# Optimization experiments

Measured on AMD Instinct MI355X. Metric: run time of the kernel, lower is better.

Reference implementation:

```python
import jax, jax.numpy as jnp
import numpy as np

N, E, C, NB, NE, G = 20000, 320000, 64, 8, 4, 16
L2 = 9          # (max_ell+1)^2 with max_ell=2
RMAX = 5.0
HID = 16        # nonlinear readout hidden width


def setup_inputs():
    key = jax.random.key(0)
    ks = jax.random.split(key, 16)
    positions = jax.random.uniform(ks[0], (N, 3), dtype=jnp.float32) * 3.0
    elems = jax.random.randint(ks[1], (N,), 0, NE)
    node_attrs = jax.nn.one_hot(elems, NE, dtype=jnp.float32)
    edge_index = jax.random.randint(ks[2], (2, E), 0, N)
    batch = jnp.sort(jax.random.randint(ks[3], (N,), 0, G))
    shifts = jnp.zeros((E, 3), jnp.float32)
    atomic_energies = jnp.array([-1.0, -2.0, -3.0, -4.0], jnp.float32)
    sc = lambda k, shp, fan: jax.random.normal(k, shp, jnp.float32) / np.sqrt(fan).astype(np.float32)
    W_embed = sc(ks[4], (NE, C), NE)
    W_up = sc(ks[5], (2, C, C), C)
    W1 = sc(ks[6], (2, NB, 64), NB)
    W2 = sc(ks[7], (2, 64, C), 64)
    W_out = sc(ks[8], (2, C, C), C)
    W_skip = sc(ks[9], (2, NE, C), NE)
    w_read0 = sc(ks[10], (C,), C)
    W_r1 = sc(ks[11], (C, HID), C)
    w_r2 = sc(ks[12], (HID,), HID)
    return dict(positions=positions, node_attrs=node_attrs, shifts=shifts,
                atomic_energies=atomic_energies, W_embed=W_embed, W_up=W_up,
                W1=W1, W2=W2, W_out=W_out, W_skip=W_skip, w_read0=w_read0,
                W_r1=W_r1, w_r2=w_r2, edge_index=edge_index, batch=batch)


def _sph_harm_l2(u):
    # component-normalized real spherical harmonics up to l=2 on unit vectors
    x, y, z = u[:, 0], u[:, 1], u[:, 2]
    s3, s5, s15 = jnp.sqrt(3.0), jnp.sqrt(5.0), jnp.sqrt(15.0)
    return jnp.stack([jnp.ones_like(x),
                      s3 * x, s3 * y, s3 * z,
                      s15 * x * y, s15 * y * z, 0.5 * s5 * (3.0 * z * z - 1.0),
                      s15 * x * z, 0.5 * s15 * (x * x - y * y)], axis=-1)


def _radial(r):
    # Bessel radial basis with polynomial cutoff (p=6)
    n = jnp.arange(1, NB + 1, dtype=jnp.float32)
    rb = jnp.sqrt(2.0 / RMAX) * jnp.sin(n * jnp.pi * r[:, None] / RMAX) / r[:, None]
    u = r / RMAX
    fc = 1.0 - 28.0 * u**6 + 48.0 * u**7 - 21.0 * u**8
    fc = jnp.where(u < 1.0, fc, 0.0)
    return rb * fc[:, None]


def _energy_contributions(positions, node_attrs, shifts, atomic_energies,
                          W_embed, W_up, W1, W2, W_out, W_skip,
                          w_read0, W_r1, w_r2, edge_index, batch):
    snd, rcv = edge_index[0], edge_index[1]
    vec = positions[snd] - positions[rcv] + shifts                  # [E,3]
    r = jnp.sqrt(jnp.sum(vec * vec, axis=-1) + 1e-12)               # [E]
    Y = _sph_harm_l2(vec / r[:, None])                              # [E,L2]
    ef = _radial(r)                                                 # [E,NB]
    # E0: per-element reference energies, summed per graph
    e0 = jax.ops.segment_sum(node_attrs @ atomic_energies, batch, num_segments=G)
    h0 = node_attrs @ W_embed                                       # [N,C] scalar feats
    h = jnp.zeros((positions.shape[0], L2, C), h0.dtype).at[:, 0, :].set(h0)
    readouts = [lambda s: s @ w_read0,
                lambda s: jax.nn.silu(s @ W_r1) @ w_r2]             # linear / nonlinear
    energies = [e0]
    for i in range(2):
        hu = jnp.einsum('nlc,cd->nld', h, W_up[i])                  # channel mix
        R = jax.nn.silu(ef @ W1[i]) @ W2[i]                         # radial MLP [E,C]
        s = jnp.einsum('elc,el->ec', hu[snd], Y)                    # equivariant contraction
        m = Y[:, :, None] * (R * s)[:, None, :]                     # [E,L2,C] messages
        agg = jax.ops.segment_sum(m, rcv, num_segments=positions.shape[0])
        h = jnp.einsum('nlc,cd->nld', agg, W_out[i])
        h = h.at[:, 0, :].add(node_attrs @ W_skip[i])               # scalar skip connection
        node_en = readouts[i](h[:, 0, :])                           # [N]
        energies.append(jax.ops.segment_sum(node_en, batch, num_segments=G))
    return jnp.stack(energies, axis=-1)                             # [G, num_interactions+1]


def reference(positions, node_attrs, shifts, atomic_energies, W_embed, W_up,
              W1, W2, W_out, W_skip, w_read0, W_r1, w_r2, edge_index, batch):
    contributions = _energy_contributions(positions, node_attrs, shifts,
        atomic_energies, W_embed, W_up, W1, W2, W_out, W_skip,
        w_read0, W_r1, w_r2, edge_index, batch)
    total_energy = jnp.sum(contributions, axis=-1)                  # [G]
    forces = -jax.grad(lambda p: jnp.sum(_energy_contributions(p, node_attrs,
        shifts, atomic_energies, W_embed, W_up, W1, W2, W_out, W_skip,
        w_read0, W_r1, w_r2, edge_index, batch)))(positions)        # [N,3]
    return total_energy, contributions, forces
```

## Files before the change

### kernel.cpp

```cpp
#include <hip/hip_runtime.h>
#include <cmath>

constexpr int N_  = 20000;
constexpr int E_  = 320000;
constexpr int NE_ = 4;
constexpr int G_  = 16;
constexpr int CAP = 96;
constexpr int TAB = 4096;
constexpr float RMAXF = 5.0f;
constexpr float PI_F  = 3.14159265358979323846f;
constexpr float S3  = 1.7320508075688772f;
constexpr float S5  = 2.2360679774997896f;
constexpr float S15 = 3.8729833462074170f;
constexpr float KC_ = 0.6324555320336759f;

typedef unsigned short u16;
typedef unsigned int   u32;
typedef _Float16 f16;
typedef _Float16 f16x2 __attribute__((ext_vector_type(2)));

#define DEV static __device__ __forceinline__

__device__ float g_fallback[110000000];

DEV float sigmoidf_(float x){ return 1.0f/(1.0f+__expf(-x)); }

DEV float b2f(u16 u){ return __uint_as_float(((u32)u)<<16); }
DEV u16  f2b(float f){
  u32 x = __float_as_uint(f);
  return (u16)((x + 0x7FFFu + ((x>>16)&1u)) >> 16);
}
DEV u16  f2h(float f){ union{f16 h; u16 u;} v; v.h=(f16)f; return v.u; }
DEV float h2f(u16 u){ union{u16 u2; f16 h;} v; v.u2=u; return (float)v.h; }

DEV f16x2 u2h(u32 x){ union{u32 u; f16x2 h;} v; v.u=x; return v.h; }
DEV u32 h2u(f16x2 h){ union{u32 u; f16x2 h;} v; v.h=h; return v.u; }
DEV u32 pkh(float a, float b){ f16x2 h; h.x=(f16)a; h.y=(f16)b; return h2u(h); }

DEV void ld4(const float* __restrict__ p, float* d){
  float4 a = ((const float4*)p)[0];
  d[0]=a.x; d[1]=a.y; d[2]=a.z; d[3]=a.w;
}
DEV void ld4b(const u16* __restrict__ p, float* d){
  ushort4 a = *(const ushort4*)p;
  d[0]=b2f(a.x); d[1]=b2f(a.y); d[2]=b2f(a.z); d[3]=b2f(a.w);
}
DEV void ld4h(const u16* __restrict__ p, float* d){
  ushort4 a = *(const ushort4*)p;
  d[0]=h2f(a.x); d[1]=h2f(a.y); d[2]=h2f(a.z); d[3]=h2f(a.w);
}
DEV void st8b(u16* p, const float* d){
  uint4 v;
  v.x = (u32)f2b(d[0]) | ((u32)f2b(d[1])<<16);
  v.y = (u32)f2b(d[2]) | ((u32)f2b(d[3])<<16);
  v.z = (u32)f2b(d[4]) | ((u32)f2b(d[5])<<16);
  v.w = (u32)f2b(d[6]) | ((u32)f2b(d[7])<<16);
  *(uint4*)p = v;
}
DEV void st8h(u16* p, const float* d){
  uint4 v;
  v.x = pkh(d[0],d[1]); v.y = pkh(d[2],d[3]);
  v.z = pkh(d[4],d[5]); v.w = pkh(d[6],d[7]);
  *(uint4*)p = v;
}

__global__ void k_cnt(const int* __restrict__ ei, int* __restrict__ cntR){
  int e = blockIdx.x*256 + threadIdx.x;
  atomicAdd(&cntR[ei[E_+e]], 1);
}

__global__ void k_scan(const int* __restrict__ cntR, int* __restrict__ offR){
  __shared__ int part[256];
  int t = threadIdx.x;
  constexpr int CH = (N_+255)/256;
  int base = t*CH;
  int s=0;
  for (int i=0;i<CH;++i){ int idx=base+i; if(idx<N_) s+=cntR[idx]; }
  part[t]=s; __syncthreads();
  for (int d=1; d<256; d<<=1){
    int v = (t>=d)? part[t-d] : 0;
    __syncthreads();
    part[t]+=v;
    __syncthreads();
  }
  int run = (t==0)?0:part[t-1];
  for (int i=0;i<CH;++i){ int idx=base+i; if(idx<N_){ offR[idx]=run; run+=cntR[idx]; } }
  if (t==255) offR[N_]=run;
}

__global__ void k_perm(const int* __restrict__ ei, const int* __restrict__ offR,
                       int* __restrict__ cntR2, int* __restrict__ cntS,
                       int* __restrict__ pe, int* __restrict__ pSnd, int* __restrict__ pRcv,
                       int* __restrict__ listS){
  int e = blockIdx.x*256 + threadIdx.x;
  int s = ei[e], r = ei[E_+e];
  int p = offR[r] + atomicAdd(&cntR2[r], 1);
  pe[p] = e; pSnd[p] = s; pRcv[p] = r;
  int q = atomicAdd(&cntS[s], 1); if (q < CAP) listS[s*CAP+q] = p;
}

__global__ void k_pre(const float* __restrict__ Wout0, const float* __restrict__ Wup1,
                      const float* __restrict__ Wskip0, const float* __restrict__ wread0,
                      float* __restrict__ WA, float* __restrict__ sa,
                      float* __restrict__ va, float* __restrict__ sv){
  int t = threadIdx.x;
  for (int idx=t; idx<4096; idx+=256){
    int c = idx>>6, d = idx&63;
    float acc=0.f;
    for (int m=0;m<64;++m) acc += Wout0[c*64+m]*Wup1[m*64+d];
    WA[idx]=acc;
  }
  {
    int k = t>>6, d = t&63;
    float acc=0.f;
    for (int m=0;m<64;++m) acc += Wskip0[k*64+m]*Wup1[m*64+d];
    sa[t]=acc;
  }
  if (t<64){
    float acc=0.f;
    for (int d=0;d<64;++d) acc += Wout0[t*64+d]*wread0[d];
    va[t]=acc;
  }
  if (t<4){
    float acc=0.f;
    for (int d=0;d<64;++d) acc += Wskip0[t*64+d]*wread0[d];
    sv[t]=acc;
  }
}

__global__ __launch_bounds__(256, 2)
void k_rtab(const float* __restrict__ W1g, const float* __restrict__ W2g,
            u16* __restrict__ tab){
  __shared__ float sW1[1024];
  __shared__ u32   sW2h[4096];
  __shared__ u32   sAh[32*36];
  int t = threadIdx.x;
  for (int i=t;i<1024;i+=256) sW1[i]=W1g[i];
  for (int i=t;i<4096;i+=256){
    int L = i>>11, rem = i&2047, kp = rem>>6, c = rem&63;
    sW2h[i] = pkh(W2g[L*4096 + (2*kp)*64 + c], W2g[L*4096 + (2*kp+1)*64 + c]);
  }
  __syncthreads();
  int wid=t>>6, lane=t&63, q=lane>>3, j=lane&7, c0=j*8;
  int slot = wid*8 + q;
  int knot = blockIdx.x*32 + slot;
  bool valid = (knot <= TAB);
  float rad = fmaxf((float)knot * (RMAXF/(float)TAB), 1e-6f);
  float inv = 1.0f/rad;
  float tt = rad*(1.0f/RMAXF);
  float fc = 0.0f, dfc = 0.0f;
  if (tt < 1.0f){
    float t2=tt*tt, t4=t2*t2, t5=t4*tt, t6=t5*tt, t7=t6*tt, t8=t7*tt;
    fc  = 1.0f - 28.0f*t6 + 48.0f*t7 - 21.0f*t8;
    dfc = (-168.0f*t5 + 336.0f*t6 - 168.0f*t7)*(1.0f/RMAXF);
  }
  float th = rad*(PI_F/RMAXF);
  float s1 = __sinf(th), c1 = __cosf(th);
  float base = KC_*inv*fc;
  float efv[8], gfv[8];
  {
    float sb = s1, cb = c1;
    #pragma unroll
    for (int b=0;b<8;++b){
      efv[b] = base*sb;
      float wb_ = (float)(b+1)*(PI_F/RMAXF);
      float rb  = KC_*sb*inv;
      float drb = KC_*(wb_*cb - sb*inv)*inv;
      gfv[b] = drb*fc + rb*dfc;
      float sn = sb*c1 + cb*s1;
      cb = cb*c1 - sb*s1;
      sb = sn;
    }
  }
  u32* myAh = sAh + slot*36;
  for (int L=0; L<2; ++L){
    const float* w1 = sW1 + L*512;
    const u32*  w2h = sW2h + L*2048;
    float zz[8]={0,0,0,0,0,0,0,0};
    float wgv[8]={0,0,0,0,0,0,0,0};
    #pragma unroll 4
    for (int b=0;b<8;++b){
      float efb = efv[b], gfb = gfv[b];
      const float4* w=(const float4*)(w1 + b*64 + c0);
      float4 wa=w[0], wb=w[1];
      zz[0]+=efb*wa.x; zz[1]+=efb*wa.y; zz[2]+=efb*wa.z; zz[3]+=efb*wa.w;
      zz[4]+=efb*wb.x; zz[5]+=efb*wb.y; zz[6]+=efb*wb.z; zz[7]+=efb*wb.w;
      wgv[0]+=gfb*wa.x; wgv[1]+=gfb*wa.y; wgv[2]+=gfb*wa.z; wgv[3]+=gfb*wa.w;
      wgv[4]+=gfb*wb.x; wgv[5]+=gfb*wb.y; wgv[6]+=gfb*wb.z; wgv[7]+=gfb*wb.w;
    }
    float a[8], dv[8];
    #pragma unroll
    for (int i=0;i<8;++i){
      float sg = sigmoidf_(zz[i]);
      a[i]  = zz[i]*sg;
      float sp = sg*(1.0f + zz[i]*(1.0f - sg));
      dv[i] = wgv[i]*sp;
    }
    {
      uint4 av;
      av.x = pkh(a[0],a[1]); av.y = pkh(a[2],a[3]);
      av.z = pkh(a[4],a[5]); av.w = pkh(a[6],a[7]);
      *(uint4*)(myAh + 4*j) = av;
    }
    {
      float r0=0.f,r1=0.f,r2=0.f,r3=0.f,r4=0.f,r5=0.f,r6=0.f,r7=0.f;
      #pragma unroll 2
      for (int kp4=0; kp4<8; ++kp4){
        uint4 dq = *(const uint4*)(myAh + 4*kp4);
        #pragma unroll
        for (int i=0;i<4;++i){
          u32 du = (i==0)?dq.x:(i==1)?dq.y:(i==2)?dq.z:dq.w;
          f16x2 dh = u2h(du);
          const u32* wrow = w2h + (4*kp4+i)*64 + c0;
          uint4 w0 = *(const uint4*)(wrow);
          uint4 w1v = *(const uint4*)(wrow+4);
          r0 = __builtin_amdgcn_fdot2(dh, u2h(w0.x),  r0, false);
          r1 = __builtin_amdgcn_fdot2(dh, u2h(w0.y),  r1, false);
          r2 = __builtin_amdgcn_fdot2(dh, u2h(w0.z),  r2, false);
          r3 = __builtin_amdgcn_fdot2(dh, u2h(w0.w),  r3, false);
          r4 = __builtin_amdgcn_fdot2(dh, u2h(w1v.x), r4, false);
          r5 = __builtin_amdgcn_fdot2(dh, u2h(w1v.y), r5, false);
          r6 = __builtin_amdgcn_fdot2(dh, u2h(w1v.z), r6, false);
          r7 = __builtin_amdgcn_fdot2(dh, u2h(w1v.w), r7, false);
        }
      }
      float racc[8] = {r0,r1,r2,r3,r4,r5,r6,r7};
      if (valid) st8h(tab + (size_t)knot*256 + L*64 + c0, racc);
    }
    {
      uint4 av;
      av.x = pkh(dv[0],dv[1]); av.y = pkh(dv[2],dv[3]);
      av.z = pkh(dv[4],dv[5]); av.w = pkh(dv[6],dv[7]);
      *(uint4*)(myAh + 4*j) = av;
    }
    {
      float r0=0.f,r1=0.f,r2=0.f,r3=0.f,r4=0.f,r5=0.f,r6=0.f,r7=0.f;
      #pragma unroll 2
      for (int kp4=0; kp4<8; ++kp4){
        uint4 dq = *(const uint4*)(myAh + 4*kp4);
        #pragma unroll
        for (int i=0;i<4;++i){
          u32 du = (i==0)?dq.x:(i==1)?dq.y:(i==2)?dq.z:dq.w;
          f16x2 dh = u2h(du);
          const u32* wrow = w2h + (4*kp4+i)*64 + c0;
          uint4 w0 = *(const uint4*)(wrow);
          uint4 w1v = *(const uint4*)(wrow+4);
          r0 = __builtin_amdgcn_fdot2(dh, u2h(w0.x),  r0, false);
          r1 = __builtin_amdgcn_fdot2(dh, u2h(w0.y),  r1, false);
          r2 = __builtin_amdgcn_fdot2(dh, u2h(w0.z),  r2, false);
          r3 = __builtin_amdgcn_fdot2(dh, u2h(w0.w),  r3, false);
          r4 = __builtin_amdgcn_fdot2(dh, u2h(w1v.x), r4, false);
          r5 = __builtin_amdgcn_fdot2(dh, u2h(w1v.y), r5, false);
          r6 = __builtin_amdgcn_fdot2(dh, u2h(w1v.z), r6, false);
          r7 = __builtin_amdgcn_fdot2(dh, u2h(w1v.w), r7, false);
        }
      }
      float qacc[8] = {r0,r1,r2,r3,r4,r5,r6,r7};
      if (valid) st8h(tab + (size_t)knot*256 + 128 + L*64 + c0, qacc);
    }
  }
}

__global__ void k_fwd_edge(const float* __restrict__ pos, const float* __restrict__ shifts,
                const int* __restrict__ pe, const int* __restrict__ pSnd,
                const int* __restrict__ pRcv, const u16* __restrict__ tab,
                float* __restrict__ Y, float* __restrict__ u3,
                float* __restrict__ irr,
                u16* __restrict__ R0, u16* __restrict__ R1,
                u16* __restrict__ q0, u16* __restrict__ q1){
  int t = threadIdx.x;
  int wid=t>>6, lane=t&63, q=lane>>3, j=lane&7, c0=j*8;
  int slot = wid*8 + q;
  int e = blockIdx.x*32 + slot;
  int eo  = pe[e];
  int snd = pSnd[e], rcv = pRcv[e];
  float vx = pos[snd*3+0]-pos[rcv*3+0]+shifts[(size_t)eo*3+0];
  float vy = pos[snd*3+1]-pos[rcv*3+1]+shifts[(size_t)eo*3+1];
  float vz = pos[snd*3+2]-pos[rcv*3+2]+shifts[(size_t)eo*3+2];
  float ss = vx*vx+vy*vy+vz*vz + 1e-12f;
  float rad = sqrtf(ss);
  float inv = 1.0f/rad;
  float x = vx*inv, y = vy*inv, z = vz*inv;
  if (j==0){
    irr[e]=inv;
    u3[(size_t)e*3+0]=x; u3[(size_t)e*3+1]=y; u3[(size_t)e*3+2]=z;
    float* Ye = Y + (size_t)e*9;
    Ye[0]=1.0f;
    Ye[1]=S3*x; Ye[2]=S3*y; Ye[3]=S3*z;
    Ye[4]=S15*x*y; Ye[5]=S15*y*z;
    Ye[6]=0.5f*S5*(3.0f*z*z-1.0f);
    Ye[7]=S15*x*z;
    Ye[8]=0.5f*S15*(x*x-y*y);
  }
  float vR0[8], vR1[8], vq0[8], vq1[8];
  if (rad < RMAXF){
    float xi = rad * ((float)TAB/RMAXF);
    int i0 = (int)xi; if (i0 > TAB-1) i0 = TAB-1;
    float f = xi - (float)i0;
    float g = 1.0f - f;
    const u16* ra = tab + (size_t)i0*256 + c0;
    const u16* rb = ra + 256;
    #pragma unroll
    for (int sec=0; sec<4; ++sec){
      ushort4 a0 = *(const ushort4*)(ra + sec*64);
      ushort4 a1 = *(const ushort4*)(ra + sec*64 + 4);
      ushort4 b0 = *(const ushort4*)(rb + sec*64);
      ushort4 b1 = *(const ushort4*)(rb + sec*64 + 4);
      float* dst = (sec==0)?vR0:(sec==1)?vR1:(sec==2)?vq0:vq1;
      dst[0]=h2f(a0.x)*g+h2f(b0.x)*f; dst[1]=h2f(a0.y)*g+h2f(b0.y)*f;
      dst[2]=h2f(a0.z)*g+h2f(b0.z)*f; dst[3]=h2f(a0.w)*g+h2f(b0.w)*f;
      dst[4]=h2f(a1.x)*g+h2f(b1.x)*f; dst[5]=h2f(a1.y)*g+h2f(b1.y)*f;
      dst[6]=h2f(a1.z)*g+h2f(b1.z)*f; dst[7]=h2f(a1.w)*g+h2f(b1.w)*f;
    }
  } else {
    #pragma unroll
    for (int i=0;i<8;++i){ vR0[i]=0.f; vR1[i]=0.f; vq0[i]=0.f; vq1[i]=0.f; }
  }
  st8b(R0 + (size_t)e*64 + c0, vR0);
  st8b(R1 + (size_t)e*64 + c0, vR1);
  st8h(q0 + (size_t)e*64 + c0, vq0);
  st8h(q1 + (size_t)e*64 + c0, vq1);
}

__global__ void k_e0(const float* __restrict__ attrs, const float* __restrict__ ae,
                     const int* __restrict__ batch, float* __restrict__ out){
  __shared__ float bins[G_];
  int t = threadIdx.x;
  if (t < G_) bins[t] = 0.f;
  __syncthreads();
  int n = blockIdx.x*256 + t;
  if (n < N_){
    float v = 0.f;
    #pragma unroll
    for (int k=0;k<NE_;++k) v += attrs[n*NE_+k]*ae[k];
    atomicAdd(&bins[batch[n]], v);
  }
  __syncthreads();
  if (t < G_){
    float b = bins[t];
    if (b != 0.f){
      atomicAdd(&out[t], b);
      atomicAdd(&out[G_ + t*3 + 0], b);
    }
  }
}

__global__ void k_wembup(const float* __restrict__ Wemb, const float* __restrict__ Wup0,
                         float* __restrict__ WembUp){
  int t = threadIdx.x; int k = t>>6, c = t&63;
  float acc = 0.f;
  for (int j=0;j<64;++j) acc += Wemb[k*64+j]*Wup0[j*64+c];
  WembUp[k*64+c] = acc;
}

__global__ void k_hu0(const float* __restrict__ attrs, const float* __restrict__ WembUp,
                      float* __restrict__ hu0){
  int i = blockIdx.x*256 + threadIdx.x;
  int n = i>>6, c = i&63;
  float acc = 0.f;
  #pragma unroll
  for (int k=0;k<NE_;++k) acc += attrs[n*NE_+k]*WembUp[k*64+c];
  hu0[i] = acc;
}

__global__ void k_agg0(const int* __restrict__ offR, const int* __restrict__ pSnd,
                       const float* __restrict__ hu0,
                       const u16* __restrict__ R0, const float* __restrict__ Y,
                       float* __restrict__ agg0){
  int t = threadIdx.x; int n = blockIdx.x*4 + (t>>6); int c = t&63;
  float acc[9] = {0,0,0,0,0,0,0,0,0};
  int p0 = offR[n], p1 = offR[n+1];
  for (int p=p0;p<p1;++p){
    int s = pSnd[p];
    float v = b2f(R0[(size_t)p*64+c])*hu0[(size_t)s*64+c];
    #pragma unroll
    for (int l=0;l<9;++l) acc[l] += Y[(size_t)p*9+l]*v;
  }
  #pragma unroll
  for (int l=0;l<9;++l) agg0[((size_t)n*9+l)*64+c] = acc[l];
}

__global__ void k_s1(const int* __restrict__ cntS, const int* __restrict__ listS,
                     const u16* __restrict__ hu1, const float* __restrict__ Y,
                     u16* __restrict__ s1){
  int t = threadIdx.x; int n = blockIdx.x*4 + (t>>6); int c = t&63;
  float hu[9];
  #pragma unroll
  for (int l=0;l<9;++l) hu[l] = b2f(hu1[((size_t)n*9+l)*64+c]);
  int deg = min(cntS[n], CAP);
  #pragma unroll 2
  for (int j=0;j<deg;++j){
    int p = listS[n*CAP+j];
    float acc = 0.f;
    #pragma unroll
    for (int l=0;l<9;++l) acc += hu[l]*Y[(size_t)p*9+l];
    s1[(size_t)p*64+c] = f2h(acc);
  }
}

__global__ void k_agg1(const int* __restrict__ offR,
                       const u16* __restrict__ R1, const u16* __restrict__ s1,
                       float* __restrict__ agg1){
  int t = threadIdx.x; int n = blockIdx.x*4 + (t>>6); int c = t&63;
  float acc = 0.f;
  int p0 = offR[n], p1 = offR[n+1];
  for (int p=p0;p<p1;++p){
    acc += b2f(R1[(size_t)p*64+c])*h2f(s1[(size_t)p*64+c]);
  }
  agg1[(size_t)n*64+c] = acc;
}

__global__ void k_dhu1(const int* __restrict__ cntS, const int* __restrict__ listS,
                       const int* __restrict__ pRcv, const u16* __restrict__ R1,
                       const float* __restrict__ ga1, const float* __restrict__ Y,
                       float* __restrict__ dhu1){
  int t = threadIdx.x; int n = blockIdx.x*4 + (t>>6); int c = t&63;
  float acc[9] = {0,0,0,0,0,0,0,0,0};
  int deg = min(cntS[n], CAP);
  #pragma unroll 2
  for (int j=0;j<deg;++j){
    int p = listS[n*CAP+j];
    int r = pRcv[p];
    float ds = b2f(R1[(size_t)p*64+c])*ga1[(size_t)r*64+c];
    #pragma unroll
    for (int l=0;l<9;++l) acc[l] += Y[(size_t)p*9+l]*ds;
  }
  #pragma unroll
  for (int l=0;l<9;++l) dhu1[((size_t)n*9+l)*64+c] = acc[l];
}

template<bool TRANS, bool OUTB>
__global__ __launch_bounds__(256, 2)
void k_mm64(const float* __restrict__ in, const float* __restrict__ W,
            void* __restrict__ out, int rows, int lper,
            const float* __restrict__ attrs, const float* __restrict__ Wsk,
            const float* __restrict__ bias){
  __shared__ float sWT[64*68];
  __shared__ float sRow[4*68];
  int t = threadIdx.x;
  for (int i=t;i<4096;i+=256){
    int k=i&63, c=i>>6;
    sWT[c*68+k] = TRANS ? W[c*64+k] : W[k*64+c];
  }
  __syncthreads();
  int wid = t>>6, c = t&63;
  float wcol[64];
  {
    const float4* wp = (const float4*)(sWT + c*68);
    #pragma unroll
    for (int kk=0;kk<16;++kk){
      float4 w4 = wp[kk];
      wcol[4*kk+0]=w4.x; wcol[4*kk+1]=w4.y; wcol[4*kk+2]=w4.z; wcol[4*kk+3]=w4.w;
    }
  }
  float* myRow = sRow + wid*68;
  for (int it=0; it<8; ++it){
    int row = (blockIdx.x*8+it)*4 + wid;
    myRow[c] = in[(size_t)row*64+c];
    float acc = 0.f;
    #pragma unroll
    for (int kk=0;kk<16;++kk){
      float4 r4 = ((const float4*)myRow)[kk];
      acc += r4.x*wcol[4*kk+0] + r4.y*wcol[4*kk+1] + r4.z*wcol[4*kk+2] + r4.w*wcol[4*kk+3];
    }
    if (lper==1 || (row % 9)==0){
      int n = (lper==1) ? row : (row/9);
      if (attrs){
        #pragma unroll
        for (int k=0;k<NE_;++k) acc += attrs[n*NE_+k]*Wsk[k*64+c];
      }
      if (bias) acc += bias[c];
    }
    if (OUTB) ((u16*)out)[(size_t)row*64+c] = f2b(acc);
    else      ((float*)out)[(size_t)row*64+c] = acc;
  }
}

__global__ void k_read0(const float* __restrict__ agg0, const float* __restrict__ va,
                        const float* __restrict__ sv, const float* __restrict__ attrs,
                        const int* __restrict__ batch, float* __restrict__ out){
  __shared__ float bins[G_];
  int t = threadIdx.x;
  if (t < G_) bins[t] = 0.f;
  __syncthreads();
  int lane = t & 63, wid = t >> 6;
  int grp = lane >> 3, j = lane & 7;
  int n = blockIdx.x*32 + wid*8 + grp;
  const float* hp = agg0 + (size_t)n*576 + j*8;
  const float* wp = va + j*8;
  float4 h0 = ((const float4*)hp)[0], h4 = ((const float4*)hp)[1];
  float4 w0v = ((const float4*)wp)[0], w4v = ((const float4*)wp)[1];
  float v = h0.x*w0v.x + h0.y*w0v.y + h0.z*w0v.z + h0.w*w0v.w
          + h4.x*w4v.x + h4.y*w4v.y + h4.z*w4v.z + h4.w*w4v.w;
  v += __shfl_xor(v,1,64); v += __shfl_xor(v,2,64); v += __shfl_xor(v,4,64);
  if (j==0){
    v += attrs[n*NE_+0]*sv[0] + attrs[n*NE_+1]*sv[1]
       + attrs[n*NE_+2]*sv[2] + attrs[n*NE_+3]*sv[3];
    atomicAdd(&bins[batch[n]], v);
  }
  __syncthreads();
  if (t < G_){
    float b = bins[t];
    if (b != 0.f){
      atomicAdd(&out[t], b);
      atomicAdd(&out[G_ + t*3 + 1], b);
    }
  }
}

__global__ void k_read1(const float* __restrict__ h2, const float* __restrict__ Wr1,
                        const float* __restrict__ wr2, const int* __restrict__ batch,
                        float* __restrict__ spz, float* __restrict__ out){
  __shared__ float sW[64*16];
  __shared__ float sA[256];
  __shared__ float bins[G_];
  int t = threadIdx.x;
  for (int i=t;i<1024;i+=256) sW[i]=Wr1[i];
  if (t < G_) bins[t] = 0.f;
  __syncthreads();
  int n = blockIdx.x*16 + (t>>4); int j = t&15;
  float z = 0.f;
  #pragma unroll 16
  for (int c=0;c<64;++c) z += h2[(size_t)n*64+c]*sW[c*16+j];
  float sg = sigmoidf_(z);
  float a  = z*sg;
  float sp = sg*(1.0f + z*(1.0f - sg));
  float w2v = wr2[j];
  spz[n*16+j] = sp*w2v;
  sA[t] = a*w2v;
  __syncthreads();
  if (j==0){
    float s = 0.f;
    #pragma unroll
    for (int k=0;k<16;++k) s += sA[t+k];
    atomicAdd(&bins[batch[n]], s);
  }
  __syncthreads();
  if (t < G_){
    float b = bins[t];
    if (b != 0.f){
      atomicAdd(&out[t], b);
      atomicAdd(&out[G_ + t*3 + 2], b);
    }
  }
}

__global__ void k_dh2(const float* __restrict__ Wr1, const float* __restrict__ spz,
                      float* __restrict__ dh2){
  int i = blockIdx.x*256 + threadIdx.x;
  int n = i>>6, c = i&63;
  float acc = 0.f;
  #pragma unroll
  for (int j=0;j<16;++j) acc += Wr1[c*16+j]*spz[n*16+j];
  dh2[i] = acc;
}

__global__ __launch_bounds__(256, 4)
void k_bedge_all(const int* __restrict__ pSnd, const int* __restrict__ pRcv,
             const float* __restrict__ Y,
             const float* __restrict__ u3, const float* __restrict__ irr,
             const u16* __restrict__ R0b, const u16* __restrict__ R1b,
             const float* __restrict__ ga1, const u16* __restrict__ ga0,
             const float* __restrict__ hu0, const u16* __restrict__ hu1,
             const u16* __restrict__ q0b, const u16* __restrict__ q1b,
             float* __restrict__ gF){
  int t = threadIdx.x;
  int wid=t>>6, lane=t&63, q=lane>>4, j=lane&15, c0=j*4;
  int slot = wid*4+q;
  int e = blockIdx.x*16 + slot;
  int snd = pSnd[e], rcv = pRcv[e];
  float Yl[9];
  #pragma unroll
  for (int l=0;l<9;++l) Yl[l] = Y[(size_t)e*9+l];
  ushort4 huv1[9];
  #pragma unroll
  for (int l=0;l<9;++l) huv1[l] = *(const ushort4*)(hu1 + ((size_t)snd*9 + l)*64 + c0);
  ushort4 gv0[9];
  #pragma unroll
  for (int l=0;l<9;++l) gv0[l] = *(const ushort4*)(ga0 + ((size_t)rcv*9 + l)*64 + c0);
  float T1[4];  ld4(ga1 + (size_t)rcv*64 + c0, T1);
  float hu0v[4]; ld4(hu0 + (size_t)snd*64 + c0, hu0v);
  float R1v[4]; ld4b(R1b + (size_t)e*64 + c0, R1v);
  float R0v[4]; ld4b(R0b + (size_t)e*64 + c0, R0v);
  float q1v[4]; ld4h(q1b + (size_t)e*64 + c0, q1v);
  float q0v[4]; ld4h(q0b + (size_t)e*64 + c0, q0v);
  float dyp[9];
  float dR1[4];
  {
    float ds1[4], sA[4];
    #pragma unroll
    for (int i=0;i<4;++i){ ds1[i]=R1v[i]*T1[i]; sA[i]=0.f; }
    #pragma unroll
    for (int l=0;l<9;++l){
      float h0v=b2f(huv1[l].x), h1v=b2f(huv1[l].y), h2v=b2f(huv1[l].z), h3v=b2f(huv1[l].w);
      float Ylv = Yl[l];
      sA[0]+=h0v*Ylv; sA[1]+=h1v*Ylv; sA[2]+=h2v*Ylv; sA[3]+=h3v*Ylv;
      dyp[l] = ds1[0]*h0v + ds1[1]*h1v + ds1[2]*h2v + ds1[3]*h3v;
    }
    #pragma unroll
    for (int i=0;i<4;++i) dR1[i]=sA[i]*T1[i];
  }
  float dR0[4];
  {
    float P[4], T0[4];
    #pragma unroll
    for (int i=0;i<4;++i){ P[i]=R0v[i]*hu0v[i]; T0[i]=0.f; }
    #pragma unroll
    for (int l=0;l<9;++l){
      float g0=b2f(gv0[l].x), g1=b2f(gv0[l].y), g2=b2f(gv0[l].z), g3=b2f(gv0[l].w);
      float Ylv = Yl[l];
      T0[0]+=g0*Ylv; T0[1]+=g1*Ylv; T0[2]+=g2*Ylv; T0[3]+=g3*Ylv;
      dyp[l] += g0*P[0] + g1*P[1] + g2*P[2] + g3*P[3];
    }
    #pragma unroll
    for (int i=0;i<4;++i) dR0[i]=hu0v[i]*T0[i];
  }
  float dy[9];
  #pragma unroll
  for (int l=1;l<9;++l){
    float v=dyp[l];
    v += __shfl_xor(v,1,64); v += __shfl_xor(v,2,64);
    v += __shfl_xor(v,4,64); v += __shfl_xor(v,8,64);
    dy[l]=v;
  }
  float dr = q1v[0]*dR1[0]+q1v[1]*dR1[1]+q1v[2]*dR1[2]+q1v[3]*dR1[3]
           + q0v[0]*dR0[0]+q0v[1]*dR0[1]+q0v[2]*dR0[2]+q0v[3]*dR0[3];
  dr += __shfl_xor(dr,1,64); dr += __shfl_xor(dr,2,64);
  dr += __shfl_xor(dr,4,64); dr += __shfl_xor(dr,8,64);
  float x = u3[(size_t)e*3+0], y = u3[(size_t)e*3+1], zz = u3[(size_t)e*3+2];
  float invr = irr[e];
  float dux = S3*dy[1] + S15*(y*dy[4] + zz*dy[7] + x*dy[8]);
  float duy = S3*dy[2] + S15*(x*dy[4] + zz*dy[5] - y*dy[8]);
  float duz = S3*dy[3] + S15*(y*dy[5] + x*dy[7]) + 3.0f*S5*zz*dy[6];
  float udot = x*dux + y*duy + zz*duz;
  float gx = dr*x + invr*(dux - x*udot);
  float gy = dr*y + invr*(duy - y*udot);
  float gz = dr*zz + invr*(duz - zz*udot);
  if (j==0){
    float* gp2 = gF + (size_t)e*3;
    gp2[0]=gx; gp2[1]=gy; gp2[2]=gz;
  }
}

__global__ void k_fsum(const int* __restrict__ offR, const int* __restrict__ cntS,
                       const int* __restrict__ listS,
                       const float* __restrict__ gF, float* __restrict__ F){
  int t = threadIdx.x;
  int lane = t & 63, wid = t >> 6;
  int sub = lane >> 3, j = lane & 7;
  int n = blockIdx.x*32 + wid*8 + sub;
  float fx=0.f, fy=0.f, fz=0.f;
  int p0 = offR[n], p1 = offR[n+1];
  for (int p=p0+j; p<p1; p+=8){
    fx += gF[(size_t)p*3+0]; fy += gF[(size_t)p*3+1]; fz += gF[(size_t)p*3+2];
  }
  int dSn = min(cntS[n], CAP);
  for (int k=j;k<dSn;k+=8){
    int p = listS[n*CAP+k];
    fx -= gF[(size_t)p*3+0]; fy -= gF[(size_t)p*3+1]; fz -= gF[(size_t)p*3+2];
  }
  fx += __shfl_xor(fx,1,64); fy += __shfl_xor(fy,1,64); fz += __shfl_xor(fz,1,64);
  fx += __shfl_xor(fx,2,64); fy += __shfl_xor(fy,2,64); fz += __shfl_xor(fz,2,64);
  fx += __shfl_xor(fx,4,64); fy += __shfl_xor(fy,4,64); fz += __shfl_xor(fz,4,64);
  if (j==0){
    F[n*3+0]=fx; F[n*3+1]=fy; F[n*3+2]=fz;
  }
}

extern "C" void kernel_launch(void* const* d_in, const int* in_sizes, int n_in,
                              void* d_out, int out_size, void* d_ws, size_t ws_size,
                              hipStream_t stream){
  (void)in_sizes; (void)n_in;
  const float* pos    = (const float*)d_in[0];
  const float* attrs  = (const float*)d_in[1];
  const float* shifts = (const float*)d_in[2];
  const float* ae     = (const float*)d_in[3];
  const float* Wemb   = (const float*)d_in[4];
  const float* Wup    = (const float*)d_in[5];
  const float* W1     = (const float*)d_in[6];
  const float* W2     = (const float*)d_in[7];
  const float* Wout   = (const float*)d_in[8];
  const float* Wskip  = (const float*)d_in[9];
  const float* wread0 = (const float*)d_in[10];
  const float* Wr1    = (const float*)d_in[11];
  const float* wr2    = (const float*)d_in[12];
  const int*   ei     = (const int*)d_in[13];
  const int*   batch  = (const int*)d_in[14];
  float* out = (float*)d_out;

  const size_t NEED = 430000000;
  char* base;
  if (ws_size >= NEED){
    base = (char*)d_ws;
  } else {
    void* p = nullptr;
    hipGetSymbolAddress(&p, HIP_SYMBOL(g_fallback));
    base = (char*)p;
  }
  size_t off = 0;
  auto alloc = [&](size_t bytes)->char*{
    char* p = base + off;
    off += ((bytes + 255)/256)*256;
    return p;
  };
  float* Y    = (float*)alloc((size_t)E_*9*4);
  float* u3   = (float*)alloc((size_t)E_*3*4);
  float* irr  = (float*)alloc((size_t)E_*4);
  u16*   R0   = (u16*)  alloc((size_t)E_*64*2);
  u16*   R1   = (u16*)  alloc((size_t)E_*64*2);
  u16*   q0   = (u16*)  alloc((size_t)E_*64*2);
  u16*   q1   = (u16*)  alloc((size_t)E_*64*2);
  u16*   s1b  = (u16*)  alloc((size_t)E_*64*2);
  float* gF   = (float*)alloc((size_t)E_*3*4);
  u16*   tab  = (u16*)  alloc((size_t)(TAB+1)*256*2);
  float* hu0  = (float*)alloc((size_t)N_*64*4);
  u16*   hu1  = (u16*)  alloc((size_t)N_*9*64*2);
  float* agg0 = (float*)alloc((size_t)N_*9*64*4);
  float* agg1 = (float*)alloc((size_t)N_*64*4);
  float* h2   = (float*)alloc((size_t)N_*64*4);
  float* spz  = (float*)alloc((size_t)N_*16*4);
  float* dh2  = (float*)alloc((size_t)N_*64*4);
  float* ga1  = (float*)alloc((size_t)N_*64*4);
  u16*   ga0  = (u16*)  alloc((size_t)N_*9*64*2);
  float* WembUp = (float*)alloc(256*4);
  float* WA   = (float*)alloc(4096*4);
  float* sa   = (float*)alloc(256*4);
  float* va   = (float*)alloc(64*4);
  float* sv   = (float*)alloc(4*4);
  int* cnts  = (int*)alloc((size_t)3*N_*4);
  int* offR  = (int*)alloc((size_t)(N_+1)*4);
  int* pe    = (int*)alloc((size_t)E_*4);
  int* pSnd  = (int*)alloc((size_t)E_*4);
  int* pRcv  = (int*)alloc((size_t)E_*4);
  int* listS = (int*)alloc((size_t)N_*CAP*4);
  int* cntR = cnts;  int* cntS = cnts + N_;  int* cntR2 = cnts + 2*N_;
  float* dhu1 = agg0;
  float* F = out + G_ + G_*3;

  hipMemsetAsync(d_out, 0, (size_t)out_size*sizeof(float), stream);
  hipMemsetAsync(cnts, 0, (size_t)3*N_*sizeof(int), stream);

  k_cnt     <<<E_/256, 256, 0, stream>>>(ei, cntR);
  k_scan    <<<1, 256, 0, stream>>>(cntR, offR);
  k_perm    <<<E_/256, 256, 0, stream>>>(ei, offR, cntR2, cntS, pe, pSnd, pRcv, listS);

  k_rtab    <<<(TAB+1+31)/32, 256, 0, stream>>>(W1, W2, tab);
  k_fwd_edge<<<E_/32, 256, 0, stream>>>(pos, shifts, pe, pSnd, pRcv, tab, Y, u3, irr, R0, R1, q0, q1);
  k_wembup  <<<1, 256, 0, stream>>>(Wemb, Wup, WembUp);
  k_pre     <<<1, 256, 0, stream>>>(Wout, Wup + 4096, Wskip, wread0, WA, sa, va, sv);
  k_e0      <<<(N_+255)/256, 256, 0, stream>>>(attrs, ae, batch, out);
  k_hu0     <<<N_*64/256, 256, 0, stream>>>(attrs, WembUp, hu0);
  k_agg0    <<<N_/4, 256, 0, stream>>>(offR, pSnd, hu0, R0, Y, agg0);
  k_mm64<false,true><<<N_*9/32, 256, 0, stream>>>(agg0, WA, hu1, N_*9, 9, attrs, sa, nullptr);
  k_read0   <<<N_/32, 256, 0, stream>>>(agg0, va, sv, attrs, batch, out);
  k_s1      <<<N_/4, 256, 0, stream>>>(cntS, listS, hu1, Y, s1b);
  k_agg1    <<<N_/4, 256, 0, stream>>>(offR, R1, s1b, agg1);
  k_mm64<false,false><<<N_/32, 256, 0, stream>>>(agg1, Wout + 4096, h2, N_, 1, attrs, Wskip + 256, nullptr);
  k_read1   <<<N_/16, 256, 0, stream>>>(h2, Wr1, wr2, batch, spz, out);

  k_dh2     <<<N_*64/256, 256, 0, stream>>>(Wr1, spz, dh2);
  k_mm64<true,false><<<N_/32, 256, 0, stream>>>(dh2, Wout + 4096, ga1, N_, 1, nullptr, nullptr, nullptr);
  k_dhu1    <<<N_/4, 256, 0, stream>>>(cntS, listS, pRcv, R1, ga1, Y, dhu1);
  k_mm64<true,true><<<N_*9/32, 256, 0, stream>>>(dhu1, WA, ga0, N_*9, 9, nullptr, nullptr, va);
  k_bedge_all<<<E_/16, 256, 0, stream>>>(pSnd, pRcv, Y, u3, irr, R0, R1, ga1, ga0, hu0, hu1, q0, q1, gF);
  k_fsum    <<<N_/32, 256, 0, stream>>>(offR, cntS, listS, gF, F);
}
```

Before: 771.3 us.

## Recompute radial features from lookup table in consumers instead of materializing per-edge

Stops writing the per-edge R0, R1, q0 and q1 feature arrays (four E×64 half-precision buffers) in the forward edge kernel. That kernel now stores only a scaled radius index per edge, and each consumer interpolates the needed values directly from the small radial lookup table. This removes a large amount of HBM write and read traffic in exchange for extra interpolation arithmetic and table gathers in the aggregation and backward kernels. The radial values R0 and R1 now stay at fp16 table precision instead of being rounded to bf16.

```diff
diff --git a/kernel.cpp b/kernel.cpp
--- a/kernel.cpp
+++ b/kernel.cpp
@@ -45,23 +45,15 @@
   ushort4 a = *(const ushort4*)p;
   d[0]=b2f(a.x); d[1]=b2f(a.y); d[2]=b2f(a.z); d[3]=b2f(a.w);
 }
-DEV void ld4h(const u16* __restrict__ p, float* d){
-  ushort4 a = *(const ushort4*)p;
-  d[0]=h2f(a.x); d[1]=h2f(a.y); d[2]=h2f(a.z); d[3]=h2f(a.w);
-}
-DEV void st8b(u16* p, const float* d){
-  uint4 v;
-  v.x = (u32)f2b(d[0]) | ((u32)f2b(d[1])<<16);
-  v.y = (u32)f2b(d[2]) | ((u32)f2b(d[3])<<16);
-  v.z = (u32)f2b(d[4]) | ((u32)f2b(d[5])<<16);
-  v.w = (u32)f2b(d[6]) | ((u32)f2b(d[7])<<16);
-  *(uint4*)p = v;
-}
 DEV void st8h(u16* p, const float* d){
   uint4 v;
   v.x = pkh(d[0],d[1]); v.y = pkh(d[2],d[3]);
   v.z = pkh(d[4],d[5]); v.w = pkh(d[6],d[7]);
   *(uint4*)p = v;
+}
+
+DEV float tlerp(const u16* __restrict__ tab, int i0, float f, int idx){
+  return h2f(tab[i0*256+idx])*(1.0f-f) + h2f(tab[(i0+1)*256+idx])*f;
 }
 
 __global__ void k_cnt(const int* __restrict__ ei, int* __restrict__ cntR){
@@ -263,15 +255,10 @@
 
 __global__ void k_fwd_edge(const float* __restrict__ pos, const float* __restrict__ shifts,
                 const int* __restrict__ pe, const int* __restrict__ pSnd,
-                const int* __restrict__ pRcv, const u16* __restrict__ tab,
+                const int* __restrict__ pRcv,
                 float* __restrict__ Y, float* __restrict__ u3,
-                float* __restrict__ irr,
-                u16* __restrict__ R0, u16* __restrict__ R1,
-                u16* __restrict__ q0, u16* __restrict__ q1){
-  int t = threadIdx.x;
-  int wid=t>>6, lane=t&63, q=lane>>3, j=lane&7, c0=j*8;
-  int slot = wid*8 + q;
-  int e = blockIdx.x*32 + slot;
+                float* __restrict__ irr, float* __restrict__ xi){
+  int e = blockIdx.x*256 + threadIdx.x;
   int eo  = pe[e];
   int snd = pSnd[e], rcv = pRcv[e];
   float vx = pos[snd*3+0]-pos[rcv*3+0]+shifts[(size_t)eo*3+0];
@@ -281,45 +268,16 @@
   float rad = sqrtf(ss);
   float inv = 1.0f/rad;
   float x = vx*inv, y = vy*inv, z = vz*inv;
-  if (j==0){
-    irr[e]=inv;
-    u3[(size_t)e*3+0]=x; u3[(size_t)e*3+1]=y; u3[(size_t)e*3+2]=z;
-    float* Ye = Y + (size_t)e*9;
-    Ye[0]=1.0f;
-    Ye[1]=S3*x; Ye[2]=S3*y; Ye[3]=S3*z;
-    Ye[4]=S15*x*y; Ye[5]=S15*y*z;
-    Ye[6]=0.5f*S5*(3.0f*z*z-1.0f);
-    Ye[7]=S15*x*z;
-    Ye[8]=0.5f*S15*(x*x-y*y);
-  }
-  float vR0[8], vR1[8], vq0[8], vq1[8];
-  if (rad < RMAXF){
-    float xi = rad * ((float)TAB/RMAXF);
-    int i0 = (int)xi; if (i0 > TAB-1) i0 = TAB-1;
-    float f = xi - (float)i0;
-    float g = 1.0f - f;
-    const u16* ra = tab + (size_t)i0*256 + c0;
-    const u16* rb = ra + 256;
-    #pragma unroll
-    for (int sec=0; sec<4; ++sec){
-      ushort4 a0 = *(const ushort4*)(ra + sec*64);
-      ushort4 a1 = *(const ushort4*)(ra + sec*64 + 4);
-      ushort4 b0 = *(const ushort4*)(rb + sec*64);
-      ushort4 b1 = *(const ushort4*)(rb + sec*64 + 4);
-      float* dst = (sec==0)?vR0:(sec==1)?vR1:(sec==2)?vq0:vq1;
-      dst[0]=h2f(a0.x)*g+h2f(b0.x)*f; dst[1]=h2f(a0.y)*g+h2f(b0.y)*f;
-      dst[2]=h2f(a0.z)*g+h2f(b0.z)*f; dst[3]=h2f(a0.w)*g+h2f(b0.w)*f;
-      dst[4]=h2f(a1.x)*g+h2f(b1.x)*f; dst[5]=h2f(a1.y)*g+h2f(b1.y)*f;
-      dst[6]=h2f(a1.z)*g+h2f(b1.z)*f; dst[7]=h2f(a1.w)*g+h2f(b1.w)*f;
-    }
-  } else {
-    #pragma unroll
-    for (int i=0;i<8;++i){ vR0[i]=0.f; vR1[i]=0.f; vq0[i]=0.f; vq1[i]=0.f; }
-  }
-  st8b(R0 + (size_t)e*64 + c0, vR0);
-  st8b(R1 + (size_t)e*64 + c0, vR1);
-  st8h(q0 + (size_t)e*64 + c0, vq0);
-  st8h(q1 + (size_t)e*64 + c0, vq1);
+  irr[e]=inv;
+  xi[e] = rad * ((float)TAB/RMAXF);
+  u3[(size_t)e*3+0]=x; u3[(size_t)e*3+1]=y; u3[(size_t)e*3+2]=z;
+  float* Ye = Y + (size_t)e*9;
+  Ye[0]=1.0f;
+  Ye[1]=S3*x; Ye[2]=S3*y; Ye[3]=S3*z;
+  Ye[4]=S15*x*y; Ye[5]=S15*y*z;
+  Ye[6]=0.5f*S5*(3.0f*z*z-1.0f);
+  Ye[7]=S15*x*z;
+  Ye[8]=0.5f*S15*(x*x-y*y);
 }
 
 __global__ void k_e0(const float* __restrict__ attrs, const float* __restrict__ ae,
@@ -365,14 +323,21 @@
 
 __global__ void k_agg0(const int* __restrict__ offR, const int* __restrict__ pSnd,
                        const float* __restrict__ hu0,
-                       const u16* __restrict__ R0, const float* __restrict__ Y,
+                       const u16* __restrict__ tab, const float* __restrict__ xi,
+                       const float* __restrict__ Y,
                        float* __restrict__ agg0){
   int t = threadIdx.x; int n = blockIdx.x*4 + (t>>6); int c = t&63;
   float acc[9] = {0,0,0,0,0,0,0,0,0};
   int p0 = offR[n], p1 = offR[n+1];
   for (int p=p0;p<p1;++p){
     int s = pSnd[p];
-    float v = b2f(R0[(size_t)p*64+c])*hu0[(size_t)s*64+c];
+    float xiv = xi[p];
+    float r0v = 0.f;
+    if (xiv < (float)TAB){
+      int i0 = (int)xiv; float f = xiv - (float)i0;
+      r0v = tlerp(tab, i0, f, c);
+    }
+    float v = r0v*hu0[(size_t)s*64+c];
     #pragma unroll
     for (int l=0;l<9;++l) acc[l] += Y[(size_t)p*9+l]*v;
   }
@@ -399,19 +364,27 @@
 }
 
 __global__ void k_agg1(const int* __restrict__ offR,
-                       const u16* __restrict__ R1, const u16* __restrict__ s1,
+                       const u16* __restrict__ tab, const float* __restrict__ xi,
+                       const u16* __restrict__ s1,
                        float* __restrict__ agg1){
   int t = threadIdx.x; int n = blockIdx.x*4 + (t>>6); int c = t&63;
   float acc = 0.f;
   int p0 = offR[n], p1 = offR[n+1];
   for (int p=p0;p<p1;++p){
-    acc += b2f(R1[(size_t)p*64+c])*h2f(s1[(size_t)p*64+c]);
+    float xiv = xi[p];
+    float r1v = 0.f;
+    if (xiv < (float)TAB){
+      int i0 = (int)xiv; float f = xiv - (float)i0;
+      r1v = tlerp(tab, i0, f, 64 + c);
+    }
+    acc += r1v*h2f(s1[(size_t)p*64+c]);
   }
   agg1[(size_t)n*64+c] = acc;
 }
 
 __global__ void k_dhu1(const int* __restrict__ cntS, const int* __restrict__ listS,
-                       const int* __restrict__ pRcv, const u16* __restrict__ R1,
+                       const int* __restrict__ pRcv,
+                       const u16* __restrict__ tab, const float* __restrict__ xi,
                        const float* __restrict__ ga1, const float* __restrict__ Y,
                        float* __restrict__ dhu1){
   int t = threadIdx.x; int n = blockIdx.x*4 + (t>>6); int c = t&63;
@@ -421,7 +394,13 @@
   for (int j=0;j<deg;++j){
     int p = listS[n*CAP+j];
     int r = pRcv[p];
-    float ds = b2f(R1[(size_t)p*64+c])*ga1[(size_t)r*64+c];
+    float xiv = xi[p];
+    float r1v = 0.f;
+    if (xiv < (float)TAB){
+      int i0 = (int)xiv; float f = xiv - (float)i0;
+      r1v = tlerp(tab, i0, f, 64 + c);
+    }
+    float ds = r1v*ga1[(size_t)r*64+c];
     #pragma unroll
     for (int l=0;l<9;++l) acc[l] += Y[(size_t)p*9+l]*ds;
   }
@@ -559,10 +538,9 @@
 void k_bedge_all(const int* __restrict__ pSnd, const int* __restrict__ pRcv,
              const float* __restrict__ Y,
              const float* __restrict__ u3, const float* __restrict__ irr,
-             const u16* __restrict__ R0b, const u16* __restrict__ R1b,
+             const u16* __restrict__ tab, const float* __restrict__ xi,
              const float* __restrict__ ga1, const u16* __restrict__ ga0,
              const float* __restrict__ hu0, const u16* __restrict__ hu1,
-             const u16* __restrict__ q0b, const u16* __restrict__ q1b,
              float* __restrict__ gF){
   int t = threadIdx.x;
   int wid=t>>6, lane=t&63, q=lane>>4, j=lane&15, c0=j*4;
@@ -580,10 +558,29 @@
   for (int l=0;l<9;++l) gv0[l] = *(const ushort4*)(ga0 + ((size_t)rcv*9 + l)*64 + c0);
   float T1[4];  ld4(ga1 + (size_t)rcv*64 + c0, T1);
   float hu0v[4]; ld4(hu0 + (size_t)snd*64 + c0, hu0v);
-  float R1v[4]; ld4b(R1b + (size_t)e*64 + c0, R1v);
-  float R0v[4]; ld4b(R0b + (size_t)e*64 + c0, R0v);
-  float q1v[4]; ld4h(q1b + (size_t)e*64 + c0, q1v);
-  float q0v[4]; ld4h(q0b + (size_t)e*64 + c0, q0v);
+  float xiv = xi[e];
+  float R0v[4], R1v[4], q0v[4], q1v[4];
+  if (xiv < (float)TAB){
+    int i0 = (int)xiv; float f = xiv - (float)i0, g = 1.0f - f;
+    const u16* ra = tab + (size_t)i0*256;
+    const u16* rb = ra + 256;
+    ushort4 a, b;
+    a = *(const ushort4*)(ra + c0);        b = *(const ushort4*)(rb + c0);
+    R0v[0]=h2f(a.x)*g+h2f(b.x)*f; R0v[1]=h2f(a.y)*g+h2f(b.y)*f;
+    R0v[2]=h2f(a.z)*g+h2f(b.z)*f; R0v[3]=h2f(a.w)*g+h2f(b.w)*f;
+    a = *(const ushort4*)(ra + 64 + c0);   b = *(const ushort4*)(rb + 64 + c0);
+    R1v[0]=h2f(a.x)*g+h2f(b.x)*f; R1v[1]=h2f(a.y)*g+h2f(b.y)*f;
+    R1v[2]=h2f(a.z)*g+h2f(b.z)*f; R1v[3]=h2f(a.w)*g+h2f(b.w)*f;
+    a = *(const ushort4*)(ra + 128 + c0);  b = *(const ushort4*)(rb + 128 + c0);
+    q0v[0]=h2f(a.x)*g+h2f(b.x)*f; q0v[1]=h2f(a.y)*g+h2f(b.y)*f;
+    q0v[2]=h2f(a.z)*g+h2f(b.z)*f; q0v[3]=h2f(a.w)*g+h2f(b.w)*f;
+    a = *(const ushort4*)(ra + 192 + c0);  b = *(const ushort4*)(rb + 192 + c0);
+    q1v[0]=h2f(a.x)*g+h2f(b.x)*f; q1v[1]=h2f(a.y)*g+h2f(b.y)*f;
+    q1v[2]=h2f(a.z)*g+h2f(b.z)*f; q1v[3]=h2f(a.w)*g+h2f(b.w)*f;
+  } else {
+    #pragma unroll
+    for (int i=0;i<4;++i){ R0v[i]=0.f; R1v[i]=0.f; q0v[i]=0.f; q1v[i]=0.f; }
+  }
   float dyp[9];
   float dR1[4];
   {
@@ -706,10 +703,7 @@
   float* Y    = (float*)alloc((size_t)E_*9*4);
   float* u3   = (float*)alloc((size_t)E_*3*4);
   float* irr  = (float*)alloc((size_t)E_*4);
-  u16*   R0   = (u16*)  alloc((size_t)E_*64*2);
-  u16*   R1   = (u16*)  alloc((size_t)E_*64*2);
-  u16*   q0   = (u16*)  alloc((size_t)E_*64*2);
-  u16*   q1   = (u16*)  alloc((size_t)E_*64*2);
+  float* xi   = (float*)alloc((size_t)E_*4);
   u16*   s1b  = (u16*)  alloc((size_t)E_*64*2);
   float* gF   = (float*)alloc((size_t)E_*3*4);
   u16*   tab  = (u16*)  alloc((size_t)(TAB+1)*256*2);
@@ -745,23 +739,23 @@
   k_perm    <<<E_/256, 256, 0, stream>>>(ei, offR, cntR2, cntS, pe, pSnd, pRcv, listS);
 
   k_rtab    <<<(TAB+1+31)/32, 256, 0, stream>>>(W1, W2, tab);
-  k_fwd_edge<<<E_/32, 256, 0, stream>>>(pos, shifts, pe, pSnd, pRcv, tab, Y, u3, irr, R0, R1, q0, q1);
+  k_fwd_edge<<<E_/256, 256, 0, stream>>>(pos, shifts, pe, pSnd, pRcv, Y, u3, irr, xi);
   k_wembup  <<<1, 256, 0, stream>>>(Wemb, Wup, WembUp);
   k_pre     <<<1, 256, 0, stream>>>(Wout, Wup + 4096, Wskip, wread0, WA, sa, va, sv);
   k_e0      <<<(N_+255)/256, 256, 0, stream>>>(attrs, ae, batch, out);
   k_hu0     <<<N_*64/256, 256, 0, stream>>>(attrs, WembUp, hu0);
-  k_agg0    <<<N_/4, 256, 0, stream>>>(offR, pSnd, hu0, R0, Y, agg0);
+  k_agg0    <<<N_/4, 256, 0, stream>>>(offR, pSnd, hu0, tab, xi, Y, agg0);
   k_mm64<false,true><<<N_*9/32, 256, 0, stream>>>(agg0, WA, hu1, N_*9, 9, attrs, sa, nullptr);
   k_read0   <<<N_/32, 256, 0, stream>>>(agg0, va, sv, attrs, batch, out);
   k_s1      <<<N_/4, 256, 0, stream>>>(cntS, listS, hu1, Y, s1b);
-  k_agg1    <<<N_/4, 256, 0, stream>>>(offR, R1, s1b, agg1);
+  k_agg1    <<<N_/4, 256, 0, stream>>>(offR, tab, xi, s1b, agg1);
   k_mm64<false,false><<<N_/32, 256, 0, stream>>>(agg1, Wout + 4096, h2, N_, 1, attrs, Wskip + 256, nullptr);
   k_read1   <<<N_/16, 256, 0, stream>>>(h2, Wr1, wr2, batch, spz, out);
 
   k_dh2     <<<N_*64/256, 256, 0, stream>>>(Wr1, spz, dh2);
   k_mm64<true,false><<<N_/32, 256, 0, stream>>>(dh2, Wout + 4096, ga1, N_, 1, nullptr, nullptr, nullptr);
-  k_dhu1    <<<N_/4, 256, 0, stream>>>(cntS, listS, pRcv, R1, ga1, Y, dhu1);
+  k_dhu1    <<<N_/4, 256, 0, stream>>>(cntS, listS, pRcv, tab, xi, ga1, Y, dhu1);
   k_mm64<true,true><<<N_*9/32, 256, 0, stream>>>(dhu1, WA, ga0, N_*9, 9, nullptr, nullptr, va);
-  k_bedge_all<<<E_/16, 256, 0, stream>>>(pSnd, pRcv, Y, u3, irr, R0, R1, ga1, ga0, hu0, hu1, q0, q1, gF);
+  k_bedge_all<<<E_/16, 256, 0, stream>>>(pSnd, pRcv, Y, u3, irr, tab, xi, ga1, ga0, hu0, hu1, gF);
   k_fsum    <<<N_/32, 256, 0, stream>>>(offR, cntS, listS, gF, F);
 }
```

After: 762.6 us. No clear change (-1.1%).
